# Kernel tuning notes

Measured on AMD Instinct MI355X. Metric: run time of the kernel, lower is better.

The kernel has to match this reference:

```python
import jax, jax.numpy as jnp
import numpy as np

N, E, G = 50000, 600000, 128
ND, ED, H, T, L = 32, 16, 128, 128, 4


def setup_inputs() -> dict:
    key = jax.random.key(0)
    ks = jax.random.split(key, 32)
    s = 0.05
    nrm = lambda k, shp: (jax.random.normal(k, shp, jnp.float32) * s)
    inp = {
        'node_f': jax.random.normal(ks[0], (N, ND), jnp.float32),
        'node_x': jax.random.normal(ks[1], (N, 3), jnp.float32),
        'edge_w': jax.random.normal(ks[2], (E, ED), jnp.float32),
        'src': jax.random.randint(ks[3], (E,), 0, N, jnp.int32),
        'dst': jax.random.randint(ks[4], (E,), 0, N, jnp.int32),
        'graph_ids': jnp.sort(jax.random.randint(ks[5], (N,), 0, G, jnp.int32)),
        'W_in': nrm(ks[6], (ND, H)), 'b_in': jnp.zeros((H,), jnp.float32),
        'W_e': nrm(ks[7], (ED, H)), 'b_e': jnp.zeros((H,), jnp.float32),
        'msg_W1': nrm(ks[8], (L, 3 * H + 1, H)), 'msg_b1': jnp.zeros((L, H), jnp.float32),
        'msg_W2': nrm(ks[9], (L, H, H)), 'msg_b2': jnp.zeros((L, H), jnp.float32),
        'upd_W1': nrm(ks[10], (L, H, H)), 'upd_b1': jnp.zeros((L, H), jnp.float32),
        'upd_W2': nrm(ks[11], (L, H, H)), 'upd_b2': jnp.zeros((L, H), jnp.float32),
        'W_out': nrm(ks[12], (2 * H, T)), 'b_out': jnp.zeros((T,), jnp.float32),
    }
    return inp


def reference(node_f, node_x, edge_w, src, dst, graph_ids,
              W_in, b_in, W_e, b_e,
              msg_W1, msg_b1, msg_W2, msg_b2,
              upd_W1, upd_b1, upd_W2, upd_b2,
              W_out, b_out):
    relu = jax.nn.relu
    # input node / edge embeddings
    f = relu(node_f @ W_in + b_in)            # [N, H]
    w = relu(edge_w @ W_e + b_e)              # [E, H]
    # squared distance per edge (positions are static across layers)
    sq = jnp.sum((node_x[src] - node_x[dst]) ** 2, axis=-1, keepdims=True)  # [E, 1]
    for i in range(L):
        mi = jnp.concatenate([f[src], f[dst], w, sq], axis=-1)  # [E, 3H+1]
        m = relu(relu(mi @ msg_W1[i] + msg_b1[i]) @ msg_W2[i] + msg_b2[i])  # [E, H]
        m_sum = jax.ops.segment_sum(m, dst, num_segments=N)     # scatter-sum to dst
        u = m_sum + f
        f = relu(relu(u @ upd_W1[i] + upd_b1[i]) @ upd_W2[i] + upd_b2[i])
    # per-graph mean / max readout
    counts = jax.ops.segment_sum(jnp.ones((N,), f.dtype), graph_ids, num_segments=G)
    mean = jax.ops.segment_sum(f, graph_ids, num_segments=G) / jnp.maximum(counts, 1.0)[:, None]
    mx = jax.ops.segment_max(f, graph_ids, num_segments=G)
    mx = jnp.where(counts[:, None] > 0, mx, 0.0)
    return jnp.concatenate([mean, mx], axis=-1) @ W_out + b_out  # [G, T]
```

## Files before the change

kernel.cpp:

```cpp
#include <hip/hip_runtime.h>
#include <hip/hip_fp16.h>

typedef _Float16 f16;
typedef _Float16 f16x8 __attribute__((ext_vector_type(8)));
typedef float f32x4 __attribute__((ext_vector_type(4)));

#define N_NODES 50000
#define N_EDGES 600000
#define G_GRAPHS 128
#define H 128
#define NP 50176
#define NT_E 18750
#define NB_E 1024
#define NT_N 1563

__global__ void k_f0(const float* __restrict__ node_f, const float* __restrict__ W_in,
                     const float* __restrict__ b_in, f16* __restrict__ fh)
{
    __shared__ float sW[32 * 128];
    __shared__ float sx[8][32];
    const int tid = threadIdx.x;
    const int base = blockIdx.x * 8;
    for (int i = tid; i < 32 * 128; i += 128) sW[i] = W_in[i];
    for (int i = tid; i < 8 * 32; i += 128) {
        int u = i >> 5, k = i & 31;
        int n = base + u;
        sx[u][k] = (n < N_NODES) ? node_f[(size_t)n * 32 + k] : 0.0f;
    }
    __syncthreads();
    const float bj = b_in[tid];
    #pragma unroll
    for (int u = 0; u < 8; ++u) {
        int n = base + u;
        if (n >= N_NODES) break;
        float acc = bj;
        #pragma unroll
        for (int k = 0; k < 32; ++k) acc = fmaf(sx[u][k], sW[k * 128 + tid], acc);
        fh[(size_t)n * H + tid] = (f16)fmaxf(acc, 0.0f);
    }
}

__global__ void k_hist(const int* __restrict__ dst, int* __restrict__ cnt)
{
    int e = blockIdx.x * 256 + threadIdx.x;
    if (e < N_EDGES) atomicAdd(&cnt[dst[e]], 1);
}

__global__ void k_scanA(const int* __restrict__ cnt, int* __restrict__ rowptr,
                        int* __restrict__ bsum)
{
    __shared__ int s[256];
    const int t = threadIdx.x;
    const int i = blockIdx.x * 256 + t;
    int v = cnt[i];
    s[t] = v;
    __syncthreads();
    #pragma unroll
    for (int off = 1; off < 256; off <<= 1) {
        int x = (t >= off) ? s[t - off] : 0;
        __syncthreads();
        s[t] += x;
        __syncthreads();
    }
    rowptr[i] = s[t] - v;
    if (t == 255) bsum[blockIdx.x] = s[255];
}

__global__ void k_scanB(const int* __restrict__ bsum, int* __restrict__ boff)
{
    __shared__ int s[256];
    const int t = threadIdx.x;
    int v = (t < 196) ? bsum[t] : 0;
    s[t] = v;
    __syncthreads();
    #pragma unroll
    for (int off = 1; off < 256; off <<= 1) {
        int x = (t >= off) ? s[t - off] : 0;
        __syncthreads();
        s[t] += x;
        __syncthreads();
    }
    boff[t] = s[t] - v;
}

__global__ void k_scanC(int* __restrict__ rowptr, const int* __restrict__ boff)
{
    int i = blockIdx.x * 256 + threadIdx.x;
    rowptr[i] += boff[blockIdx.x];
}

__global__ void k_scatter_idx(const int* __restrict__ dst, const int* __restrict__ rowptr,
                              int* __restrict__ fill, int* __restrict__ perm_eidx)
{
    int e = blockIdx.x * 256 + threadIdx.x;
    if (e >= N_EDGES) return;
    int d = dst[e];
    int p = rowptr[d] + atomicAdd(&fill[d], 1);
    perm_eidx[p] = e;
}

__global__ void k_gather(const int* __restrict__ perm_eidx, const float* __restrict__ edge_w,
                         const int* __restrict__ src, const int* __restrict__ dst,
                         const float* __restrict__ node_x,
                         int* __restrict__ perm_src, int* __restrict__ perm_dst,
                         float* __restrict__ perm_sq, f16* __restrict__ perm_ewh)
{
    int pp = blockIdx.x * 256 + threadIdx.x;
    if (pp >= N_EDGES) return;
    int e = perm_eidx[pp];
    int s = src[e], d = dst[e];
    float dx = node_x[s * 3 + 0] - node_x[d * 3 + 0];
    float dy = node_x[s * 3 + 1] - node_x[d * 3 + 1];
    float dz = node_x[s * 3 + 2] - node_x[d * 3 + 2];
    perm_src[pp] = s;
    perm_dst[pp] = d;
    perm_sq[pp] = dx * dx + dy * dy + dz * dz;
    const float4* pw = (const float4*)(edge_w + (size_t)e * 16);
    float4 w0 = pw[0], w1 = pw[1], w2 = pw[2], w3 = pw[3];
    f16x8 v0, v1;
    v0[0] = (f16)w0.x; v0[1] = (f16)w0.y; v0[2] = (f16)w0.z; v0[3] = (f16)w0.w;
    v0[4] = (f16)w1.x; v0[5] = (f16)w1.y; v0[6] = (f16)w1.z; v0[7] = (f16)w1.w;
    v1[0] = (f16)w2.x; v1[1] = (f16)w2.y; v1[2] = (f16)w2.z; v1[3] = (f16)w2.w;
    v1[4] = (f16)w3.x; v1[5] = (f16)w3.y; v1[6] = (f16)w3.z; v1[7] = (f16)w3.w;
    f16x8* q = (f16x8*)(perm_ewh + (size_t)pp * 16);
    q[0] = v0; q[1] = v1;
}

__global__ __launch_bounds__(512, 2) void k_edge2(
    const f16* __restrict__ fh,
    const int* __restrict__ perm_src, const int* __restrict__ perm_dst,
    const float* __restrict__ perm_sq, const f16* __restrict__ perm_ewh,
    const float* __restrict__ W_e, const float* __restrict__ b_e,
    const float* __restrict__ W1, const float* __restrict__ b1,
    const float* __restrict__ W2, const float* __restrict__ b2,
    f16* __restrict__ msum)
{
    const int tid = threadIdx.x;
    const int wave = tid >> 6;
    const int lane = tid & 63;
    const int l16 = lane & 15;
    const int lq  = lane >> 4;
    const int col = wave * 16 + l16;

    f16x8 wef, w1f[12], w2f[4];
    #pragma unroll
    for (int j = 0; j < 8; ++j) {
        int k = lq * 8 + j;
        wef[j] = (k < 16) ? (f16)W_e[(size_t)k * H + col] : (f16)0.0f;
    }
    #pragma unroll
    for (int k = 0; k < 12; ++k)
        #pragma unroll
        for (int j = 0; j < 8; ++j)
            w1f[k][j] = (f16)W1[(size_t)(k * 32 + lq * 8 + j) * H + col];
    #pragma unroll
    for (int k = 0; k < 4; ++k)
        #pragma unroll
        for (int j = 0; j < 8; ++j)
            w2f[k][j] = (f16)W2[(size_t)(k * 32 + lq * 8 + j) * H + col];
    const float w1last = W1[(size_t)384 * H + col];
    const float b1v = b1[col], b2v = b2[col], bev = b_e[col];

    __shared__ alignas(16) f16 Atile[2][32][392];
    __shared__ alignas(16) f16 h1B[2][32][136];
    __shared__ int   s_src[3][32];
    __shared__ int   s_dst[3][32];
    __shared__ float s_sq[3][32];

    const int b = ((blockIdx.x & 7) << 7) | (blockIdx.x >> 3);
    const int t0 = (int)((long)b * NT_E / NB_E);
    const int t1 = (int)((long)(b + 1) * NT_E / NB_E);

    const int srow = tid >> 4, sch = tid & 15;
    const int sj = ((srow >> 2) & 3) * 8 + ((srow >> 4) << 2) + (srow & 3);

    if (tid < 32) {
        int e0 = t0 * 32 + tid;
        s_src[t0 % 3][tid] = perm_src[e0];
        s_dst[t0 % 3][tid] = perm_dst[e0];
        s_sq [t0 % 3][tid] = perm_sq[e0];
        int e1 = min((t0 + 1) * 32 + tid, N_EDGES - 1);
        s_src[(t0 + 1) % 3][tid] = perm_src[e1];
        s_dst[(t0 + 1) % 3][tid] = perm_dst[e1];
        s_sq [(t0 + 1) % 3][tid] = perm_sq[e1];
    }
    __syncthreads();
    {
        const int pa = t0 & 1;
        int sv = s_src[t0 % 3][sj], dv = s_dst[t0 % 3][sj];
        int4 ra = ((const int4*)(fh + (size_t)sv * H))[sch];
        int4 rb = ((const int4*)(fh + (size_t)dv * H))[sch];
        ((int4*)&Atile[pa][srow][0])[sch]   = ra;
        ((int4*)&Atile[pa][srow][128])[sch] = rb;
        #pragma unroll
        for (int m = 0; m < 2; ++m) {
            f16x8 aa;
            if (lq < 2) {
                int j = (l16 >> 2) * 8 + m * 4 + (l16 & 3);
                aa = *(const f16x8*)(perm_ewh + (size_t)(t0 * 32 + j) * 16 + lq * 8);
            } else {
                #pragma unroll
                for (int jj = 0; jj < 8; ++jj) aa[jj] = (f16)0.0f;
            }
            f32x4 c = {bev, bev, bev, bev};
            c = __builtin_amdgcn_mfma_f32_16x16x32_f16(aa, wef, c, 0, 0, 0);
            #pragma unroll
            for (int r = 0; r < 4; ++r)
                Atile[pa][m * 16 + lq * 4 + r][256 + col] = (f16)fmaxf(c[r], 0.0f);
        }
    }
    __syncthreads();

    int dcp[8];
    for (int t = t0; t < t1; ++t) {
        const int pa = t & 1;
        const int m0 = t % 3;
        const int m1 = (t + 1) % 3;
        const int m2 = (t + 2) % 3;

        int dc[8];
        f32x4 acc1[2];
        #pragma unroll
        for (int m = 0; m < 2; ++m)
            #pragma unroll
            for (int r = 0; r < 4; ++r) {
                int j = lq * 8 + m * 4 + r;
                dc[m * 4 + r] = s_dst[m0][j];
                acc1[m][r] = fmaf(s_sq[m0][j], w1last, b1v);
            }

        int4 rs_, rd_;
        f16x8 rew[2];
        {
            int sv = s_src[m1][sj], dv = s_dst[m1][sj];
            rs_ = ((const int4*)(fh + (size_t)sv * H))[sch];
            rd_ = ((const int4*)(fh + (size_t)dv * H))[sch];
            #pragma unroll
            for (int m = 0; m < 2; ++m) {
                if (lq < 2) {
                    int j = (l16 >> 2) * 8 + m * 4 + (l16 & 3);
                    int e = min((t + 1) * 32 + j, N_EDGES - 1);
                    rew[m] = *(const f16x8*)(perm_ewh + (size_t)e * 16 + lq * 8);
                }
            }
        }
        int mrs = 0, mrd = 0; float mrq = 0.0f;
        if (tid < 32) {
            int e = min((t + 2) * 32 + tid, N_EDGES - 1);
            mrs = perm_src[e]; mrd = perm_dst[e]; mrq = perm_sq[e];
        }

        if (t > t0) {
            f32x4 acc2[2];
            #pragma unroll
            for (int m = 0; m < 2; ++m) {
                f32x4 c = {b2v, b2v, b2v, b2v};
                acc2[m] = c;
            }
            #pragma unroll
            for (int k = 0; k < 4; ++k) {
                #pragma unroll
                for (int m = 0; m < 2; ++m) {
                    f16x8 a = *(const f16x8*)&h1B[pa ^ 1][m * 16 + l16][k * 32 + lq * 8];
                    acc2[m] = __builtin_amdgcn_mfma_f32_16x16x32_f16(a, w2f[k], acc2[m], 0, 0, 0);
                }
            }
            float run = fmaxf(acc2[0][0], 0.0f);
            int cd = dcp[0];
            #pragma unroll
            for (int i = 1; i < 8; ++i) {
                float v = fmaxf(acc2[i >> 2][i & 3], 0.0f);
                int d = dcp[i];
                if (d == cd) {
                    run += v;
                } else {
                    float nb = __shfl_xor(run, 1);
                    if ((l16 & 1) == 0) {
                        union { f16 h[2]; __half2 v2; } u;
                        u.h[0] = (f16)run; u.h[1] = (f16)nb;
                        unsafeAtomicAdd((__half2*)&msum[(size_t)cd * H + col], u.v2);
                    }
                    run = v; cd = d;
                }
            }
            float nb = __shfl_xor(run, 1);
            if ((l16 & 1) == 0) {
                union { f16 h[2]; __half2 v2; } u;
                u.h[0] = (f16)run; u.h[1] = (f16)nb;
                unsafeAtomicAdd((__half2*)&msum[(size_t)cd * H + col], u.v2);
            }
        }

        #pragma unroll
        for (int k = 0; k < 12; ++k) {
            #pragma unroll
            for (int m = 0; m < 2; ++m) {
                f16x8 a = *(const f16x8*)&Atile[pa][m * 16 + l16][k * 32 + lq * 8];
                acc1[m] = __builtin_amdgcn_mfma_f32_16x16x32_f16(a, w1f[k], acc1[m], 0, 0, 0);
            }
        }
        #pragma unroll
        for (int m = 0; m < 2; ++m)
            #pragma unroll
            for (int r = 0; r < 4; ++r)
                h1B[pa][m * 16 + lq * 4 + r][col] = (f16)fmaxf(acc1[m][r], 0.0f);

        #pragma unroll
        for (int m = 0; m < 2; ++m) {
            f16x8 aa;
            if (lq < 2) {
                aa = rew[m];
            } else {
                #pragma unroll
                for (int jj = 0; jj < 8; ++jj) aa[jj] = (f16)0.0f;
            }
            f32x4 c = {bev, bev, bev, bev};
            c = __builtin_amdgcn_mfma_f32_16x16x32_f16(aa, wef, c, 0, 0, 0);
            #pragma unroll
            for (int r = 0; r < 4; ++r)
                Atile[pa ^ 1][m * 16 + lq * 4 + r][256 + col] = (f16)fmaxf(c[r], 0.0f);
        }
        ((int4*)&Atile[pa ^ 1][srow][0])[sch]   = rs_;
        ((int4*)&Atile[pa ^ 1][srow][128])[sch] = rd_;
        if (tid < 32) {
            s_src[m2][tid] = mrs; s_dst[m2][tid] = mrd; s_sq[m2][tid] = mrq;
        }
        #pragma unroll
        for (int i = 0; i < 8; ++i) dcp[i] = dc[i];
        __syncthreads();
    }

    {
        const int ph = (t1 - 1) & 1;
        f32x4 acc2[2];
        #pragma unroll
        for (int m = 0; m < 2; ++m) {
            f32x4 c = {b2v, b2v, b2v, b2v};
            acc2[m] = c;
        }
        #pragma unroll
        for (int k = 0; k < 4; ++k) {
            #pragma unroll
            for (int m = 0; m < 2; ++m) {
                f16x8 a = *(const f16x8*)&h1B[ph][m * 16 + l16][k * 32 + lq * 8];
                acc2[m] = __builtin_amdgcn_mfma_f32_16x16x32_f16(a, w2f[k], acc2[m], 0, 0, 0);
            }
        }
        float run = fmaxf(acc2[0][0], 0.0f);
        int cd = dcp[0];
        #pragma unroll
        for (int i = 1; i < 8; ++i) {
            float v = fmaxf(acc2[i >> 2][i & 3], 0.0f);
            int d = dcp[i];
            if (d == cd) {
                run += v;
            } else {
                float nb = __shfl_xor(run, 1);
                if ((l16 & 1) == 0) {
                    union { f16 h[2]; __half2 v2; } u;
                    u.h[0] = (f16)run; u.h[1] = (f16)nb;
                    unsafeAtomicAdd((__half2*)&msum[(size_t)cd * H + col], u.v2);
                }
                run = v; cd = d;
            }
        }
        float nb = __shfl_xor(run, 1);
        if ((l16 & 1) == 0) {
            union { f16 h[2]; __half2 v2; } u;
            u.h[0] = (f16)run; u.h[1] = (f16)nb;
            unsafeAtomicAdd((__half2*)&msum[(size_t)cd * H + col], u.v2);
        }
    }
}

__global__ __launch_bounds__(256, 3) void k_update(
    const f16* __restrict__ msum, f16* __restrict__ fh,
    const float* __restrict__ W1, const float* __restrict__ b1,
    const float* __restrict__ W2, const float* __restrict__ b2)
{
    const int tid = threadIdx.x;
    const int wave = tid >> 6;
    const int lane = tid & 63;
    const int l16 = lane & 15;
    const int lq = lane >> 4;
    const int colbase = wave * 32;

    f16x8 w1fr[4][2], w2fr[4][2];
    float b1v[2], b2v[2];
    #pragma unroll
    for (int nt = 0; nt < 2; ++nt) {
        const int col = colbase + nt * 16 + l16;
        #pragma unroll
        for (int k = 0; k < 4; ++k) {
            f16x8 v1, v2;
            #pragma unroll
            for (int j = 0; j < 8; ++j) {
                v1[j] = (f16)W1[(size_t)(k * 32 + lq * 8 + j) * H + col];
                v2[j] = (f16)W2[(size_t)(k * 32 + lq * 8 + j) * H + col];
            }
            w1fr[k][nt] = v1;
            w2fr[k][nt] = v2;
        }
        b1v[nt] = b1[col];
        b2v[nt] = b2[col];
    }

    __shared__ alignas(16) f16 U[32][136];
    __shared__ alignas(16) f16 h1b[32][136];
    const int row = tid >> 3, ch = tid & 7;

    int tile = blockIdx.x;
    f16x8 rm0, rm1, rf0, rf1;
    if (tile < NT_N) {
        int n = min(tile * 32 + row, N_NODES - 1);
        const f16x8* pm = (const f16x8*)(msum + (size_t)n * H) + ch * 2;
        const f16x8* pf = (const f16x8*)(fh + (size_t)n * H) + ch * 2;
        rm0 = pm[0]; rm1 = pm[1]; rf0 = pf[0]; rf1 = pf[1];
    }
    for (; tile < NT_N; tile += gridDim.x) {
        const int n0 = tile * 32;
        {
            f16 tmp[16];
            #pragma unroll
            for (int j = 0; j < 8; ++j) {
                tmp[j]     = (f16)((float)rm0[j] + (float)rf0[j]);
                tmp[8 + j] = (f16)((float)rm1[j] + (float)rf1[j]);
            }
            int4* q0 = (int4*)(&U[row][ch * 16]);
            q0[0] = ((const int4*)tmp)[0];
            q0[1] = ((const int4*)tmp)[1];
        }
        {
            int nt_ = tile + gridDim.x;
            if (nt_ < NT_N) {
                int n = min(nt_ * 32 + row, N_NODES - 1);
                const f16x8* pm = (const f16x8*)(msum + (size_t)n * H) + ch * 2;
                const f16x8* pf = (const f16x8*)(fh + (size_t)n * H) + ch * 2;
                rm0 = pm[0]; rm1 = pm[1]; rf0 = pf[0]; rf1 = pf[1];
            }
        }
        __syncthreads();

        f32x4 acc[2][2];
        #pragma unroll
        for (int m = 0; m < 2; ++m)
            #pragma unroll
            for (int nt = 0; nt < 2; ++nt) {
                f32x4 c = {b1v[nt], b1v[nt], b1v[nt], b1v[nt]};
                acc[m][nt] = c;
            }
        #pragma unroll
        for (int k = 0; k < 4; ++k) {
            #pragma unroll
            for (int m = 0; m < 2; ++m) {
                f16x8 a = *(const f16x8*)&U[m * 16 + l16][k * 32 + lq * 8];
                #pragma unroll
                for (int nt = 0; nt < 2; ++nt)
                    acc[m][nt] = __builtin_amdgcn_mfma_f32_16x16x32_f16(a, w1fr[k][nt], acc[m][nt], 0, 0, 0);
            }
        }
        #pragma unroll
        for (int m = 0; m < 2; ++m)
            #pragma unroll
            for (int nt = 0; nt < 2; ++nt)
                #pragma unroll
                for (int r = 0; r < 4; ++r)
                    h1b[m * 16 + lq * 4 + r][colbase + nt * 16 + l16] = (f16)fmaxf(acc[m][nt][r], 0.0f);
        __syncthreads();

        f32x4 acc2[2][2];
        #pragma unroll
        for (int m = 0; m < 2; ++m)
            #pragma unroll
            for (int nt = 0; nt < 2; ++nt) {
                f32x4 c = {b2v[nt], b2v[nt], b2v[nt], b2v[nt]};
                acc2[m][nt] = c;
            }
        #pragma unroll
        for (int k = 0; k < 4; ++k) {
            #pragma unroll
            for (int m = 0; m < 2; ++m) {
                f16x8 a = *(const f16x8*)&h1b[m * 16 + l16][k * 32 + lq * 8];
                #pragma unroll
                for (int nt = 0; nt < 2; ++nt)
                    acc2[m][nt] = __builtin_amdgcn_mfma_f32_16x16x32_f16(a, w2fr[k][nt], acc2[m][nt], 0, 0, 0);
            }
        }
        #pragma unroll
        for (int m = 0; m < 2; ++m)
            #pragma unroll
            for (int nt = 0; nt < 2; ++nt)
                #pragma unroll
                for (int r = 0; r < 4; ++r) {
                    int rr = m * 16 + lq * 4 + r;
                    int n = n0 + rr;
                    if (n < N_NODES)
                        fh[(size_t)n * H + colbase + nt * 16 + l16] = (f16)fmaxf(acc2[m][nt][r], 0.0f);
                }
    }
}

__global__ void k_readout(const f16* __restrict__ fh, const int* __restrict__ gid,
                          float* __restrict__ gsum, float* __restrict__ gmax,
                          int* __restrict__ gcnt)
{
    __shared__ int s_gid[64];
    const int tid = threadIdx.x;
    const int base = blockIdx.x * 64;
    if (tid < 64) s_gid[tid] = (base + tid < N_NODES) ? gid[base + tid] : -1;
    __syncthreads();
    if (tid < 64 && base + tid < N_NODES) atomicAdd(&gcnt[s_gid[tid]], 1);

    float lsum = 0.0f, lmax = 0.0f;
    int cur = s_gid[0];
    if (cur >= 0) {
        for (int i = 0; i < 64; ++i) {
            int g = s_gid[i];
            if (g < 0) break;
            if (g != cur) {
                unsafeAtomicAdd(&gsum[(size_t)cur * H + tid], lsum);
                atomicMax((int*)&gmax[(size_t)cur * H + tid], __float_as_int(lmax));
                lsum = 0.0f; lmax = 0.0f; cur = g;
            }
            float v = (float)fh[(size_t)(base + i) * H + tid];
            lsum += v;
            lmax = fmaxf(lmax, v);
        }
        unsafeAtomicAdd(&gsum[(size_t)cur * H + tid], lsum);
        atomicMax((int*)&gmax[(size_t)cur * H + tid], __float_as_int(lmax));
    }
}

__global__ void k_out(const float* __restrict__ gsum, const float* __restrict__ gmax,
                      const int* __restrict__ gcnt, const float* __restrict__ W_out,
                      const float* __restrict__ b_out, float* __restrict__ out)
{
    __shared__ float sm[128], sx[128];
    const int g = blockIdx.x, t = threadIdx.x;
    const float inv = 1.0f / fmaxf((float)gcnt[g], 1.0f);
    sm[t] = gsum[(size_t)g * H + t] * inv;
    sx[t] = gmax[(size_t)g * H + t];
    __syncthreads();
    float acc = b_out[t];
    for (int k = 0; k < H; ++k) {
        acc = fmaf(sm[k], W_out[(size_t)k * 128 + t], acc);
        acc = fmaf(sx[k], W_out[(size_t)(128 + k) * 128 + t], acc);
    }
    out[(size_t)g * 128 + t] = acc;
}

extern "C" void kernel_launch(void* const* d_in, const int* in_sizes, int n_in,
                              void* d_out, int out_size, void* d_ws, size_t ws_size,
                              hipStream_t stream)
{
    const float* node_f = (const float*)d_in[0];
    const float* node_x = (const float*)d_in[1];
    const float* edge_w = (const float*)d_in[2];
    const int*   src    = (const int*)d_in[3];
    const int*   dst    = (const int*)d_in[4];
    const int*   gid    = (const int*)d_in[5];
    const float* W_in   = (const float*)d_in[6];
    const float* b_in   = (const float*)d_in[7];
    const float* W_e    = (const float*)d_in[8];
    const float* b_e    = (const float*)d_in[9];
    const float* msg_W1 = (const float*)d_in[10];
    const float* msg_b1 = (const float*)d_in[11];
    const float* msg_W2 = (const float*)d_in[12];
    const float* msg_b2 = (const float*)d_in[13];
    const float* upd_W1 = (const float*)d_in[14];
    const float* upd_b1 = (const float*)d_in[15];
    const float* upd_W2 = (const float*)d_in[16];
    const float* upd_b2 = (const float*)d_in[17];
    const float* W_out  = (const float*)d_in[18];
    const float* b_out  = (const float*)d_in[19];
    float* out = (float*)d_out;

    char* ws = (char*)d_ws;
    size_t off = 0;
    f16*   fh       = (f16*)(ws + off);   off += (size_t)N_NODES * H * 2;
    f16*   perm_ewh = (f16*)(ws + off);   off += (size_t)N_EDGES * 16 * 2;
    int*   perm_src = (int*)(ws + off);   off += (size_t)N_EDGES * 4;
    int*   perm_dst = (int*)(ws + off);   off += (size_t)N_EDGES * 4;
    float* perm_sq  = (float*)(ws + off); off += (size_t)N_EDGES * 4;
    int*   rowptr   = (int*)(ws + off);   off += (size_t)NP * 4;
    int*   cnt      = (int*)(ws + off);   off += (size_t)NP * 4;
    int*   bsum     = (int*)(ws + off);   off += 256 * 4;
    int*   boff     = (int*)(ws + off);   off += 256 * 4;
    f16*   msum     = (f16*)(ws + off);   off += (size_t)N_NODES * H * 2;
    float* gsum     = (float*)(ws + off); off += (size_t)G_GRAPHS * H * 4;
    float* gmax     = (float*)(ws + off); off += (size_t)G_GRAPHS * H * 4;
    int*   gcnt     = (int*)(ws + off);   off += (size_t)G_GRAPHS * 4;
    int*   perm_eidx = (int*)msum;

    k_f0<<<(N_NODES + 7) / 8, 128, 0, stream>>>(node_f, W_in, b_in, fh);

    (void)hipMemsetAsync(cnt, 0, (size_t)NP * 4, stream);
    k_hist<<<(N_EDGES + 255) / 256, 256, 0, stream>>>(dst, cnt);
    k_scanA<<<NP / 256, 256, 0, stream>>>(cnt, rowptr, bsum);
    k_scanB<<<1, 256, 0, stream>>>(bsum, boff);
    k_scanC<<<NP / 256, 256, 0, stream>>>(rowptr, boff);
    (void)hipMemsetAsync(cnt, 0, (size_t)NP * 4, stream);
    k_scatter_idx<<<(N_EDGES + 255) / 256, 256, 0, stream>>>(dst, rowptr, cnt, perm_eidx);
    k_gather<<<(N_EDGES + 255) / 256, 256, 0, stream>>>(perm_eidx, edge_w, src, dst, node_x,
                                                        perm_src, perm_dst, perm_sq, perm_ewh);

    for (int l = 0; l < 4; ++l) {
        (void)hipMemsetAsync(msum, 0, (size_t)N_NODES * H * 2, stream);
        k_edge2<<<NB_E, 512, 0, stream>>>(fh, perm_src, perm_dst, perm_sq, perm_ewh,
                                          W_e, b_e,
                                          msg_W1 + (size_t)l * 385 * H, msg_b1 + (size_t)l * H,
                                          msg_W2 + (size_t)l * H * H,  msg_b2 + (size_t)l * H,
                                          msum);
        k_update<<<512, 256, 0, stream>>>(msum, fh,
                                          upd_W1 + (size_t)l * H * H, upd_b1 + (size_t)l * H,
                                          upd_W2 + (size_t)l * H * H, upd_b2 + (size_t)l * H);
    }

    (void)hipMemsetAsync(gsum, 0, (size_t)G_GRAPHS * H * 4, stream);
    (void)hipMemsetAsync(gmax, 0, (size_t)G_GRAPHS * H * 4, stream);
    (void)hipMemsetAsync(gcnt, 0, (size_t)G_GRAPHS * 4, stream);
    k_readout<<<(N_NODES + 63) / 64, 128, 0, stream>>>(fh, gid, gsum, gmax, gcnt);
    k_out<<<G_GRAPHS, 128, 0, stream>>>(gsum, gmax, gcnt, W_out, b_out, out);
}
```

Before: 1.182 ms.

## Precompute per-node src/dst projections of message W1 before edge kernel

Splits the first message-MLP matmul by linearity: a new per-node kernel computes f@W1_src and f@W1_dst once per layer, and the edge kernel gathers and sums these projections instead of gathering raw features and doing the full 384-wide K loop. This cuts the edge MFMA work for the first layer to the edge-embedding slice and shrinks shared memory, which allows higher occupancy via the launch bounds change. It adds an extra kernel launch and node-sized writes per layer, and fp16 rounding of the projections changes numerics slightly.

After: 2.404 ms. +103.4%, slower.

```diff
diff --git a/kernel.cpp b/kernel.cpp
--- a/kernel.cpp
+++ b/kernel.cpp
@@ -126,8 +126,101 @@
     q[0] = v0; q[1] = v1;
 }
 
-__global__ __launch_bounds__(512, 2) void k_edge2(
-    const f16* __restrict__ fh,
+__global__ __launch_bounds__(256, 3) void k_proj(
+    const f16* __restrict__ fh, const float* __restrict__ W1,
+    f16* __restrict__ Gs, f16* __restrict__ Gd)
+{
+    const int tid = threadIdx.x;
+    const int wave = tid >> 6;
+    const int lane = tid & 63;
+    const int l16 = lane & 15;
+    const int lq = lane >> 4;
+    const int colbase = wave * 32;
+
+    f16x8 wsa[4][2], wsb[4][2];
+    #pragma unroll
+    for (int nt = 0; nt < 2; ++nt) {
+        const int col = colbase + nt * 16 + l16;
+        #pragma unroll
+        for (int k = 0; k < 4; ++k) {
+            f16x8 va, vb;
+            #pragma unroll
+            for (int j = 0; j < 8; ++j) {
+                va[j] = (f16)W1[(size_t)(k * 32 + lq * 8 + j) * H + col];
+                vb[j] = (f16)W1[(size_t)(128 + k * 32 + lq * 8 + j) * H + col];
+            }
+            wsa[k][nt] = va;
+            wsb[k][nt] = vb;
+        }
+    }
+
+    __shared__ alignas(16) f16 U[32][136];
+    const int row = tid >> 3, ch = tid & 7;
+
+    int tile = blockIdx.x;
+    f16x8 rf0, rf1;
+    if (tile < NT_N) {
+        int n = min(tile * 32 + row, N_NODES - 1);
+        const f16x8* pf = (const f16x8*)(fh + (size_t)n * H) + ch * 2;
+        rf0 = pf[0]; rf1 = pf[1];
+    }
+    for (; tile < NT_N; tile += gridDim.x) {
+        const int n0 = tile * 32;
+        {
+            int4* q0 = (int4*)(&U[row][ch * 16]);
+            q0[0] = *(const int4*)&rf0;
+            q0[1] = *(const int4*)&rf1;
+        }
+        {
+            int nt_ = tile + gridDim.x;
+            if (nt_ < NT_N) {
+                int n = min(nt_ * 32 + row, N_NODES - 1);
+                const f16x8* pf = (const f16x8*)(fh + (size_t)n * H) + ch * 2;
+                rf0 = pf[0]; rf1 = pf[1];
+            }
+        }
+        __syncthreads();
+
+        f32x4 accs[2][2], accd[2][2];
+        #pragma unroll
+        for (int m = 0; m < 2; ++m)
+            #pragma unroll
+            for (int nt = 0; nt < 2; ++nt) {
+                f32x4 z = {0.0f, 0.0f, 0.0f, 0.0f};
+                accs[m][nt] = z; accd[m][nt] = z;
+            }
+        #pragma unroll
+        for (int k = 0; k < 4; ++k) {
+            #pragma unroll
+            for (int m = 0; m < 2; ++m) {
+                f16x8 a = *(const f16x8*)&U[m * 16 + l16][k * 32 + lq * 8];
+                #pragma unroll
+                for (int nt = 0; nt < 2; ++nt) {
+                    accs[m][nt] = __builtin_amdgcn_mfma_f32_16x16x32_f16(a, wsa[k][nt], accs[m][nt], 0, 0, 0);
+                    accd[m][nt] = __builtin_amdgcn_mfma_f32_16x16x32_f16(a, wsb[k][nt], accd[m][nt], 0, 0, 0);
+                }
+            }
+        }
+        #pragma unroll
+        for (int m = 0; m < 2; ++m)
+            #pragma unroll
+            for (int nt = 0; nt < 2; ++nt)
+                #pragma unroll
+                for (int r = 0; r < 4; ++r) {
+                    int rr = m * 16 + lq * 4 + r;
+                    int n = n0 + rr;
+                    if (n < N_NODES) {
+                        int col = colbase + nt * 16 + l16;
+                        Gs[(size_t)n * H + col] = (f16)accs[m][nt][r];
+                        Gd[(size_t)n * H + col] = (f16)accd[m][nt][r];
+                    }
+                }
+        __syncthreads();
+    }
+}
+
+__global__ __launch_bounds__(512, 6) void k_edge2(
+    const f16* __restrict__ Gs, const f16* __restrict__ Gd,
     const int* __restrict__ perm_src, const int* __restrict__ perm_dst,
     const float* __restrict__ perm_sq, const f16* __restrict__ perm_ewh,
     const float* __restrict__ W_e, const float* __restrict__ b_e,
@@ -142,27 +235,25 @@
     const int lq  = lane >> 4;
     const int col = wave * 16 + l16;
 
-    f16x8 wef, w1f[12], w2f[4];
+    f16x8 wef, w1f[4], w2f[4];
     #pragma unroll
     for (int j = 0; j < 8; ++j) {
         int k = lq * 8 + j;
         wef[j] = (k < 16) ? (f16)W_e[(size_t)k * H + col] : (f16)0.0f;
     }
     #pragma unroll
-    for (int k = 0; k < 12; ++k)
-        #pragma unroll
-        for (int j = 0; j < 8; ++j)
-            w1f[k][j] = (f16)W1[(size_t)(k * 32 + lq * 8 + j) * H + col];
-    #pragma unroll
     for (int k = 0; k < 4; ++k)
         #pragma unroll
-        for (int j = 0; j < 8; ++j)
+        for (int j = 0; j < 8; ++j) {
+            w1f[k][j] = (f16)W1[(size_t)(256 + k * 32 + lq * 8 + j) * H + col];
             w2f[k][j] = (f16)W2[(size_t)(k * 32 + lq * 8 + j) * H + col];
+        }
     const float w1last = W1[(size_t)384 * H + col];
     const float b1v = b1[col], b2v = b2[col], bev = b_e[col];
 
-    __shared__ alignas(16) f16 Atile[2][32][392];
+    __shared__ alignas(16) f16 Atile[2][32][136];
     __shared__ alignas(16) f16 h1B[2][32][136];
+    __shared__ alignas(16) f16 Gt[2][32][136];
     __shared__ int   s_src[3][32];
     __shared__ int   s_dst[3][32];
     __shared__ float s_sq[3][32];
@@ -188,10 +279,12 @@
     {
         const int pa = t0 & 1;
         int sv = s_src[t0 % 3][sj], dv = s_dst[t0 % 3][sj];
-        int4 ra = ((const int4*)(fh + (size_t)sv * H))[sch];
-        int4 rb = ((const int4*)(fh + (size_t)dv * H))[sch];
-        ((int4*)&Atile[pa][srow][0])[sch]   = ra;
-        ((int4*)&Atile[pa][srow][128])[sch] = rb;
+        union { int4 i; f16x8 h; } ua, ub, uo;
+        ua.i = ((const int4*)(Gs + (size_t)sv * H))[sch];
+        ub.i = ((const int4*)(Gd + (size_t)dv * H))[sch];
+        #pragma unroll
+        for (int j = 0; j < 8; ++j) uo.h[j] = (f16)((float)ua.h[j] + (float)ub.h[j]);
+        ((int4*)&Gt[pa][srow][0])[sch] = uo.i;
         #pragma unroll
         for (int m = 0; m < 2; ++m) {
             f16x8 aa;
@@ -206,7 +299,7 @@
             c = __builtin_amdgcn_mfma_f32_16x16x32_f16(aa, wef, c, 0, 0, 0);
             #pragma unroll
             for (int r = 0; r < 4; ++r)
-                Atile[pa][m * 16 + lq * 4 + r][256 + col] = (f16)fmaxf(c[r], 0.0f);
+                Atile[pa][m * 16 + lq * 4 + r][col] = (f16)fmaxf(c[r], 0.0f);
         }
     }
     __syncthreads();
@@ -225,16 +318,17 @@
             #pragma unroll
             for (int r = 0; r < 4; ++r) {
                 int j = lq * 8 + m * 4 + r;
+                int row = m * 16 + lq * 4 + r;
                 dc[m * 4 + r] = s_dst[m0][j];
-                acc1[m][r] = fmaf(s_sq[m0][j], w1last, b1v);
-            }
-
-        int4 rs_, rd_;
+                acc1[m][r] = fmaf(s_sq[m0][j], w1last, b1v) + (float)Gt[pa][row][col];
+            }
+
+        int4 ga_, gb_;
         f16x8 rew[2];
         {
             int sv = s_src[m1][sj], dv = s_dst[m1][sj];
-            rs_ = ((const int4*)(fh + (size_t)sv * H))[sch];
-            rd_ = ((const int4*)(fh + (size_t)dv * H))[sch];
+            ga_ = ((const int4*)(Gs + (size_t)sv * H))[sch];
+            gb_ = ((const int4*)(Gd + (size_t)dv * H))[sch];
             #pragma unroll
             for (int m = 0; m < 2; ++m) {
                 if (lq < 2) {
@@ -292,7 +386,7 @@
         }
 
         #pragma unroll
-        for (int k = 0; k < 12; ++k) {
+        for (int k = 0; k < 4; ++k) {
             #pragma unroll
             for (int m = 0; m < 2; ++m) {
                 f16x8 a = *(const f16x8*)&Atile[pa][m * 16 + l16][k * 32 + lq * 8];
@@ -318,10 +412,15 @@
             c = __builtin_amdgcn_mfma_f32_16x16x32_f16(aa, wef, c, 0, 0, 0);
             #pragma unroll
             for (int r = 0; r < 4; ++r)
-                Atile[pa ^ 1][m * 16 + lq * 4 + r][256 + col] = (f16)fmaxf(c[r], 0.0f);
-        }
-        ((int4*)&Atile[pa ^ 1][srow][0])[sch]   = rs_;
-        ((int4*)&Atile[pa ^ 1][srow][128])[sch] = rd_;
+                Atile[pa ^ 1][m * 16 + lq * 4 + r][col] = (f16)fmaxf(c[r], 0.0f);
+        }
+        {
+            union { int4 i; f16x8 h; } ua, ub, uo;
+            ua.i = ga_; ub.i = gb_;
+            #pragma unroll
+            for (int j = 0; j < 8; ++j) uo.h[j] = (f16)((float)ua.h[j] + (float)ub.h[j]);
+            ((int4*)&Gt[pa ^ 1][srow][0])[sch] = uo.i;
+        }
         if (tid < 32) {
             s_src[m2][tid] = mrs; s_dst[m2][tid] = mrd; s_sq[m2][tid] = mrq;
         }
@@ -578,6 +677,8 @@
     char* ws = (char*)d_ws;
     size_t off = 0;
     f16*   fh       = (f16*)(ws + off);   off += (size_t)N_NODES * H * 2;
+    f16*   Gs       = (f16*)(ws + off);   off += (size_t)N_NODES * H * 2;
+    f16*   Gd       = (f16*)(ws + off);   off += (size_t)N_NODES * H * 2;
     f16*   perm_ewh = (f16*)(ws + off);   off += (size_t)N_EDGES * 16 * 2;
     int*   perm_src = (int*)(ws + off);   off += (size_t)N_EDGES * 4;
     int*   perm_dst = (int*)(ws + off);   off += (size_t)N_EDGES * 4;
@@ -606,7 +707,8 @@
 
     for (int l = 0; l < 4; ++l) {
         (void)hipMemsetAsync(msum, 0, (size_t)N_NODES * H * 2, stream);
-        k_edge2<<<NB_E, 512, 0, stream>>>(fh, perm_src, perm_dst, perm_sq, perm_ewh,
+        k_proj<<<512, 256, 0, stream>>>(fh, msg_W1 + (size_t)l * 385 * H, Gs, Gd);
+        k_edge2<<<NB_E, 512, 0, stream>>>(Gs, Gd, perm_src, perm_dst, perm_sq, perm_ewh,
                                           W_e, b_e,
                                           msg_W1 + (size_t)l * 385 * H, msg_b1 + (size_t)l * H,
                                           msg_W2 + (size_t)l * H * H,  msg_b2 + (size_t)l * H,
```
